# Optimization experiments

Measured on AMD Instinct MI355X. Metric: run time of the kernel, lower is better.

Reference implementation:

```python
import jax, jax.numpy as jnp
import numpy as np

N = 50000          # nodes
E = 800000         # edges
IN = 32            # in_channels (train_tensor.shape[1])
OUT = 256          # out_channels
K = 4              # Chebyshev order
LAMBDA_MAX = 2.0   # canonical lambda_max for sym-normalized Laplacian


def setup_inputs() -> dict:
    key = jax.random.key(0)
    ks = jax.random.split(key, 32)
    inp = {}
    inp["X"] = jax.random.normal(ks[0], (N, IN), jnp.float32)
    inp["edge_index"] = jax.random.randint(ks[1], (2, E), 0, N)
    inp["edge_weight"] = jax.random.uniform(ks[2], (E,), jnp.float32)
    inp["H"] = jax.random.normal(ks[3], (N, OUT), jnp.float32)
    inp["C"] = jax.random.normal(ks[4], (N, OUT), jnp.float32)
    i = 5
    s_in = float(np.sqrt(6.0 / (IN + OUT)))   # glorot for W_g
    s_ch = float(np.sqrt(1.0 / OUT))          # ChebConv linear init scale
    for g in ["i", "f", "c", "o"]:
        inp[f"W_{g}"] = jax.random.uniform(ks[i], (IN, OUT), jnp.float32, -s_in, s_in); i += 1
        inp[f"b_{g}"] = jnp.zeros((1, OUT), jnp.float32)
        inp[f"conv_{g}_w"] = jax.random.uniform(ks[i], (K, OUT, OUT), jnp.float32, -s_ch, s_ch); i += 1
        inp[f"conv_{g}_b"] = jnp.zeros((OUT,), jnp.float32)
    return inp


def _cheb_basis(H, edge_index, edge_weight, lam):
    """Chebyshev basis T_0(L~)H .. T_{K-1}(L~)H for the scaled sym Laplacian.
    L~ = (2/lam) * (I - D^{-1/2} A D^{-1/2}) - I  (PyG ChebConv.__norm__)."""
    n = H.shape[0]
    src, dst = edge_index[0], edge_index[1]
    deg = jax.ops.segment_sum(edge_weight, src, num_segments=n)
    dis = jnp.where(deg > 0, jax.lax.rsqrt(deg), 0.0)
    w = -(2.0 / lam) * dis[src] * edge_weight * dis[dst]   # scaled off-diagonal
    d = 2.0 / lam - 1.0                                     # scaled diagonal

    def prop(x):  # L~ @ x via edge scatter + diagonal
        return jax.ops.segment_sum(w[:, None] * x[src], dst, num_segments=n) + d * x

    Tx0 = H
    Tx1 = prop(Tx0)
    Tx2 = 2.0 * prop(Tx1) - Tx0
    Tx3 = 2.0 * prop(Tx2) - Tx1
    return jnp.stack([Tx0, Tx1, Tx2, Tx3])  # [K, N, OUT]


def reference(X, edge_index, edge_weight, H, C,
              W_i, b_i, conv_i_w, conv_i_b,
              W_f, b_f, conv_f_w, conv_f_b,
              W_c, b_c, conv_c_w, conv_c_b,
              W_o, b_o, conv_o_w, conv_o_b):
    # Shared Chebyshev basis of H (identical across the 4 gates)
    Tx = _cheb_basis(H, edge_index, edge_weight, LAMBDA_MAX)  # [K, N, OUT]

    def gate(Wg, bg, cw, cb):
        conv = jnp.einsum('knf,kfo->no', Tx, cw) + cb
        return X @ Wg + conv + bg

    I = jax.nn.sigmoid(gate(W_i, b_i, conv_i_w, conv_i_b))
    F = jax.nn.sigmoid(gate(W_f, b_f, conv_f_w, conv_f_b))
    T = jnp.tanh(gate(W_c, b_c, conv_c_w, conv_c_b))
    C_new = F * C + I * T
    O = jax.nn.sigmoid(gate(W_o, b_o, conv_o_w, conv_o_b))
    H_new = O * jnp.tanh(C_new)
    return (H_new, C_new)
```

## Files before the change

### kernel.cpp

```cpp
#include <hip/hip_runtime.h>
#include <math.h>

#define NN   50000
#define EE   800000
#define INC  32
#define OUTC 256
#define NKB  132

using bf16x8 = __attribute__((ext_vector_type(8))) short;
using u16x8  = __attribute__((ext_vector_type(8))) unsigned short;
using f32x4  = __attribute__((ext_vector_type(4))) float;

struct __align__(8) Edge { int s; float w; };

__device__ __forceinline__ unsigned short f2b(float f) {
  union { float f; unsigned u; } v; v.f = f;
  return (unsigned short)((v.u + 0x7FFFu + ((v.u >> 16) & 1u)) >> 16);
}
__device__ __forceinline__ float b2f(unsigned short u) {
  union { unsigned u; float f; } v; v.u = ((unsigned)u) << 16; return v.f;
}


__global__ void k_edge1(const int* __restrict__ ei, const float* __restrict__ ew,
                        float* __restrict__ deg, int* __restrict__ cnt) {
  for (int e = blockIdx.x * blockDim.x + threadIdx.x; e < EE;
       e += gridDim.x * blockDim.x) {
    atomicAdd(&deg[ei[e]], ew[e]);
    atomicAdd(&cnt[ei[EE + e]], 1);
  }
}

__global__ __launch_bounds__(512) void k_scan1(const int* __restrict__ cnt,
                                               int* __restrict__ row_ptr,
                                               int* __restrict__ bsum) {
  __shared__ int sd[512];
  int t = threadIdx.x;
  int i = blockIdx.x * 512 + t;
  int x = (i < NN) ? cnt[i] : 0;
  sd[t] = x;
  __syncthreads();
  for (int off = 1; off < 512; off <<= 1) {
    int v = (t >= off) ? sd[t - off] : 0;
    __syncthreads();
    sd[t] += v;
    __syncthreads();
  }
  if (i < NN) row_ptr[i] = sd[t] - x;
  if (t == 511) bsum[blockIdx.x] = sd[511];
}

__global__ __launch_bounds__(128) void k_scan2(int* __restrict__ bsum,
                                               int* __restrict__ row_ptr,
                                               int nblk) {
  __shared__ int sd[128];
  int t = threadIdx.x;
  int x = (t < nblk) ? bsum[t] : 0;
  sd[t] = x;
  __syncthreads();
  for (int off = 1; off < 128; off <<= 1) {
    int v = (t >= off) ? sd[t - off] : 0;
    __syncthreads();
    sd[t] += v;
    __syncthreads();
  }
  if (t < nblk) bsum[t] = sd[t] - x;
  if (t == 127) row_ptr[NN] = sd[127];
}

__global__ void k_scan3(int* __restrict__ row_ptr, const int* __restrict__ bsum,
                        int* __restrict__ nxt, float* __restrict__ deg) {
  int i = blockIdx.x * blockDim.x + threadIdx.x;
  if (i < NN) {
    int v = row_ptr[i] + bsum[i >> 9];
    row_ptr[i] = v;
    nxt[i] = v;
    float d = deg[i];
    deg[i] = d > 0.f ? rsqrtf(d) : 0.f;
  }
}

__global__ void k_fill(const int* __restrict__ ei, const float* __restrict__ ew,
                       const float* __restrict__ dis, int* __restrict__ nxt,
                       Edge* __restrict__ ev) {
  for (int e = blockIdx.x * blockDim.x + threadIdx.x; e < EE;
       e += gridDim.x * blockDim.x) {
    int s = ei[e], d = ei[EE + e];
    int pos = atomicAdd(&nxt[d], 1);
    Edge eg; eg.s = s; eg.w = -dis[s] * ew[e] * dis[d];
    ev[pos] = eg;
  }
}


__global__ __launch_bounds__(256) void k_prop_bf(
    const int* __restrict__ row_ptr, const Edge* __restrict__ ev,
    const unsigned short* __restrict__ xb,
    const unsigned short* __restrict__ initb, float scale,
    unsigned short* __restrict__ outb) {
  int wid = blockIdx.x * 4 + (threadIdx.x >> 6);
  if (wid >= NN) return;
  int lane = threadIdx.x & 63;
  int half = lane >> 5;
  int cl = lane & 31;
  int start = __builtin_amdgcn_readfirstlane(row_ptr[wid]);
  int end = __builtin_amdgcn_readfirstlane(row_ptr[wid + 1]);
  const size_t cofs = (size_t)(cl << 3);

  float a0[8], a1[8], a2[8], a3[8];
#pragma unroll
  for (int i = 0; i < 8; ++i) { a0[i] = 0.f; a1[i] = 0.f; a2[i] = 0.f; a3[i] = 0.f; }

  int j = start;
  for (; j + 7 < end; j += 8) {
    Edge e0 = ev[j + half];
    Edge e1 = ev[j + 2 + half];
    Edge e2 = ev[j + 4 + half];
    Edge e3 = ev[j + 6 + half];
    u16x8 u0 = *(const u16x8*)(xb + (size_t)e0.s * OUTC + cofs);
    u16x8 u1 = *(const u16x8*)(xb + (size_t)e1.s * OUTC + cofs);
    u16x8 u2 = *(const u16x8*)(xb + (size_t)e2.s * OUTC + cofs);
    u16x8 u3 = *(const u16x8*)(xb + (size_t)e3.s * OUTC + cofs);
#pragma unroll
    for (int i = 0; i < 8; ++i) {
      a0[i] = fmaf(e0.w, b2f(u0[i]), a0[i]);
      a1[i] = fmaf(e1.w, b2f(u1[i]), a1[i]);
      a2[i] = fmaf(e2.w, b2f(u2[i]), a2[i]);
      a3[i] = fmaf(e3.w, b2f(u3[i]), a3[i]);
    }
  }
  for (; j + 1 < end; j += 2) {
    Edge e0 = ev[j + half];
    u16x8 u0 = *(const u16x8*)(xb + (size_t)e0.s * OUTC + cofs);
#pragma unroll
    for (int i = 0; i < 8; ++i) a0[i] = fmaf(e0.w, b2f(u0[i]), a0[i]);
  }
  if (j < end) {
    Edge e0 = ev[j];
    float wv = half ? 0.f : e0.w;
    u16x8 u0 = *(const u16x8*)(xb + (size_t)e0.s * OUTC + cofs);
#pragma unroll
    for (int i = 0; i < 8; ++i) a0[i] = fmaf(wv, b2f(u0[i]), a0[i]);
  }

  float o[8];
#pragma unroll
  for (int i = 0; i < 8; ++i) {
    float s = (a0[i] + a1[i]) + (a2[i] + a3[i]);
    s += __shfl_xor(s, 32);
    o[i] = s;
  }
  if (initb) {
    u16x8 iv = *(const u16x8*)(initb + (size_t)wid * OUTC + cofs);
#pragma unroll
    for (int i = 0; i < 8; ++i) o[i] = scale * o[i] - b2f(iv[i]);
  }
  if (half == 1) {
    u16x8 h;
#pragma unroll
    for (int i = 0; i < 8; ++i) h[i] = f2b(o[i]);
    *(u16x8*)(outb + (size_t)wid * OUTC + cofs) = h;
  }
}


__global__ void k_packXH(const float* __restrict__ X, const float* __restrict__ H,
                         unsigned short* __restrict__ xrm,
                         unsigned short* __restrict__ hrm) {
  int t = blockIdx.x * blockDim.x + threadIdx.x;
  if (t < NN * 4) {
    int row = t >> 2, kb = t & 3;
    float4 a = *(const float4*)(X + (size_t)row * INC + kb * 8);
    float4 b = *(const float4*)(X + (size_t)row * INC + kb * 8 + 4);
    u16x8 h;
    h[0] = f2b(a.x); h[1] = f2b(a.y); h[2] = f2b(a.z); h[3] = f2b(a.w);
    h[4] = f2b(b.x); h[5] = f2b(b.y); h[6] = f2b(b.z); h[7] = f2b(b.w);
    *(u16x8*)(xrm + (size_t)row * INC + kb * 8) = h;
  } else if (t < NN * 36) {
    int u = t - NN * 4;
    int row = u >> 5, kb = u & 31;
    float4 a = *(const float4*)(H + (size_t)row * OUTC + kb * 8);
    float4 b = *(const float4*)(H + (size_t)row * OUTC + kb * 8 + 4);
    u16x8 h;
    h[0] = f2b(a.x); h[1] = f2b(a.y); h[2] = f2b(a.z); h[3] = f2b(a.w);
    h[4] = f2b(b.x); h[5] = f2b(b.y); h[6] = f2b(b.z); h[7] = f2b(b.w);
    *(u16x8*)(hrm + (size_t)row * OUTC + kb * 8) = h;
  }
}

struct BPtrs {
  const float* W[4];
  const float* cw[4];
  const float* b[4];
  const float* cb[4];
};

__global__ void k_packB(BPtrs bp, unsigned short* __restrict__ bpk,
                        float* __restrict__ bias_pk) {
  int t = blockIdx.x * blockDim.x + threadIdx.x;
  if (t >= NKB * 1024) return;
  int kb = t >> 10, p = t & 1023;
  int j = p >> 7, c = (p >> 6) & 1, g = (p >> 4) & 3, s = p & 15;
  int o = j * 32 + c * 16 + s;
  u16x8 h;
#pragma unroll
  for (int j8 = 0; j8 < 8; ++j8) {
    int k = kb * 8 + j8;
    float v = (k < 32) ? bp.W[g][k * OUTC + o]
                       : bp.cw[g][(size_t)(k - 32) * OUTC + o];
    h[j8] = f2b(v);
  }
  *(u16x8*)(bpk + (size_t)t * 8) = h;
  if (kb == 0) bias_pk[p] = bp.b[g][o] + bp.cb[g][o];
}


__device__ __forceinline__ float sigf(float x) {
  return __builtin_amdgcn_rcpf(1.0f + __expf(-x));
}
__device__ __forceinline__ float tanhfast(float x) {
  float e = __expf(2.0f * x);
  return 1.0f - 2.0f * __builtin_amdgcn_rcpf(e + 1.0f);
}

#define AS1(p) ((__attribute__((address_space(1))) void*)(p))
#define AS3(p) ((__attribute__((address_space(3))) void*)(p))

__global__ __launch_bounds__(512, 6) void k_gemm_mfma(
    const unsigned short* __restrict__ Xrm,
    const unsigned short* __restrict__ Hrm,
    const unsigned short* __restrict__ T1rm,
    const unsigned short* __restrict__ T2rm,
    const unsigned short* __restrict__ T3rm,
    const unsigned short* __restrict__ Bpk,
    const float* __restrict__ bias_pk,
    const float* __restrict__ C,
    float* __restrict__ Hn, float* __restrict__ Cn) {
  __shared__ unsigned short Als[3][128 * 4 * 8];
  __shared__ unsigned short Bls[3][4 * 128 * 8];

  const int b = blockIdx.x;
  const int xcd = b & 7;
  const int slot = b >> 3;
  const int cgrp = slot & 7;
  const int rblk = xcd + ((slot >> 3) << 3);
  const int bm0 = rblk * 128;
  if (bm0 >= NN) return;
  const int cb0 = cgrp * 128;

  const int tid = threadIdx.x;
  const int lane = tid & 63;
  const int wid = tid >> 6;
  const int wr = wid >> 1;
  const int wc = wid & 1;

  f32x4 acc[2][4];
#pragma unroll
  for (int i = 0; i < 2; ++i)
#pragma unroll
    for (int j = 0; j < 4; ++j) acc[i][j] = (f32x4){0.f, 0.f, 0.f, 0.f};

  const int sr = lane >> 2;
  const int scs = (lane & 3) ^ ((sr >> 1) & 3);
  int arow = bm0 + (wid << 4) + sr;
  if (arow > NN - 1) arow = NN - 1;
  const size_t rowA32 = (size_t)arow * INC + ((size_t)scs << 3);
  const size_t rowA256 = (size_t)arow * OUTC + ((size_t)scs << 3);
  const int idxw = wid << 6;
  const unsigned short* bG =
      Bpk + (((size_t)(idxw >> 7)) * 1024 + cb0 + (idxw & 127) + lane) * 8;

  auto STAGE_A = [&](int buf, int tile) {
    const unsigned short* src;
    if (tile == 0)      src = Xrm + rowA32;
    else if (tile < 9)  src = Hrm  + rowA256 + (size_t)(tile - 1) * 32;
    else if (tile < 17) src = T1rm + rowA256 + (size_t)(tile - 9) * 32;
    else if (tile < 25) src = T2rm + rowA256 + (size_t)(tile - 17) * 32;
    else                src = T3rm + rowA256 + (size_t)(tile - 25) * 32;
    __builtin_amdgcn_global_load_lds(AS1(src),
                                     AS3(&Als[buf][wid << 9]), 16, 0, 0);
  };
  auto STAGE_B = [&](int buf, int tile) {
    __builtin_amdgcn_global_load_lds(AS1(bG + ((size_t)(tile << 2)) * 1024 * 8),
                                     AS3(&Bls[buf][(wid << 6) * 8]), 16, 0, 0);
  };

  const int koff = lane >> 4;
  const int r15 = lane & 15;
  const int NT = NKB / 4;

  STAGE_A(0, 0); STAGE_B(0, 0);
  STAGE_A(1, 1); STAGE_B(1, 1);
  int cur = 0;
  for (int t = 0; t < NT; ++t) {
    if (t < NT - 1)
      asm volatile("s_waitcnt vmcnt(2)\n\ts_barrier" ::: "memory");
    else
      asm volatile("s_waitcnt vmcnt(0)\n\ts_barrier" ::: "memory");

    const int row0 = (wr << 5) + r15;
    const int asw = (r15 >> 1) & 3;
    const unsigned short* Ab = &Als[cur][row0 * 32 + ((koff ^ asw) << 3)];
    const unsigned short* Bb = &Bls[cur][((koff << 7) + (wc << 6) + r15) * 8];

    bf16x8 af0 = *(const bf16x8*)(Ab);
    bf16x8 af1 = *(const bf16x8*)(Ab + 512);
    bf16x8 bf0 = *(const bf16x8*)(Bb + 0 * 8);
    bf16x8 bf1 = *(const bf16x8*)(Bb + 16 * 8);
    bf16x8 bf2 = *(const bf16x8*)(Bb + 32 * 8);
    bf16x8 bf3 = *(const bf16x8*)(Bb + 48 * 8);
    if (t + 2 < NT) { STAGE_A((t + 2) % 3, t + 2); STAGE_B((t + 2) % 3, t + 2); }
    __builtin_amdgcn_s_barrier();
    asm volatile("s_waitcnt lgkmcnt(0)" ::: "memory");
    __builtin_amdgcn_sched_barrier(0);
    __builtin_amdgcn_s_setprio(1);
    acc[0][0] = __builtin_amdgcn_mfma_f32_16x16x32_bf16(af0, bf0, acc[0][0], 0, 0, 0);
    acc[1][0] = __builtin_amdgcn_mfma_f32_16x16x32_bf16(af1, bf0, acc[1][0], 0, 0, 0);
    acc[0][1] = __builtin_amdgcn_mfma_f32_16x16x32_bf16(af0, bf1, acc[0][1], 0, 0, 0);
    acc[1][1] = __builtin_amdgcn_mfma_f32_16x16x32_bf16(af1, bf1, acc[1][1], 0, 0, 0);
    acc[0][2] = __builtin_amdgcn_mfma_f32_16x16x32_bf16(af0, bf2, acc[0][2], 0, 0, 0);
    acc[1][2] = __builtin_amdgcn_mfma_f32_16x16x32_bf16(af1, bf2, acc[1][2], 0, 0, 0);
    acc[0][3] = __builtin_amdgcn_mfma_f32_16x16x32_bf16(af0, bf3, acc[0][3], 0, 0, 0);
    acc[1][3] = __builtin_amdgcn_mfma_f32_16x16x32_bf16(af1, bf3, acc[1][3], 0, 0, 0);
    __builtin_amdgcn_s_setprio(0);

    cur = (cur + 1 == 3) ? 0 : cur + 1;
  }

  const int ocol = cgrp * 32 + (wc << 4) + r15;
  float bz[4];
#pragma unroll
  for (int g = 0; g < 4; ++g) bz[g] = bias_pk[cb0 + (wc << 6) + (g << 4) + r15];

#pragma unroll
  for (int mi = 0; mi < 2; ++mi) {
    int rowb = bm0 + (wr << 5) + (mi << 4) + ((lane >> 4) << 2);
#pragma unroll
    for (int q = 0; q < 4; ++q) {
      int r = rowb + q;
      if (r >= NN) continue;
      float zi = acc[mi][0][q] + bz[0];
      float zf = acc[mi][1][q] + bz[1];
      float zc = acc[mi][2][q] + bz[2];
      float zo = acc[mi][3][q] + bz[3];
      float cold = C[(size_t)r * OUTC + ocol];
      float I = sigf(zi), F = sigf(zf), T = tanhfast(zc), O = sigf(zo);
      float cn = fmaf(F, cold, I * T);
      Cn[(size_t)r * OUTC + ocol] = cn;
      Hn[(size_t)r * OUTC + ocol] = O * tanhfast(cn);
    }
  }
}


extern "C" void kernel_launch(void* const* d_in, const int* in_sizes, int n_in,
                              void* d_out, int out_size, void* d_ws, size_t ws_size,
                              hipStream_t stream) {
  const float* X = (const float*)d_in[0];
  const int* EI = (const int*)d_in[1];
  const float* EW = (const float*)d_in[2];
  const float* H = (const float*)d_in[3];
  const float* C = (const float*)d_in[4];

  char* ws = (char*)d_ws;
  size_t off = 0;
  auto alloc = [&](size_t bytes) -> void* {
    void* p = ws + off;
    off += (bytes + 255) & ~(size_t)255;
    return p;
  };
  int* row_ptr = (int*)alloc((NN + 1) * sizeof(int));
  int* cnt = (int*)alloc(NN * sizeof(int));
  int* nextp = (int*)alloc(NN * sizeof(int));
  int* bsum = (int*)alloc(128 * sizeof(int));
  Edge* ev = (Edge*)alloc(EE * sizeof(Edge));
  float* dis = (float*)alloc(NN * sizeof(float));
  unsigned short* Xrm = (unsigned short*)alloc((size_t)NN * INC * sizeof(unsigned short));
  unsigned short* Hrm = (unsigned short*)alloc((size_t)NN * OUTC * sizeof(unsigned short));
  unsigned short* T1rm = (unsigned short*)alloc((size_t)NN * OUTC * sizeof(unsigned short));
  unsigned short* T2rm = (unsigned short*)alloc((size_t)NN * OUTC * sizeof(unsigned short));
  unsigned short* T3rm = (unsigned short*)alloc((size_t)NN * OUTC * sizeof(unsigned short));
  unsigned short* Bpk = (unsigned short*)alloc((size_t)NKB * 1024 * 8 * sizeof(unsigned short));
  float* bias_pk = (float*)alloc(1024 * sizeof(float));
  (void)ws_size; (void)in_sizes; (void)n_in; (void)out_size;

  hipMemsetAsync(dis, 0, NN * sizeof(float), stream);
  hipMemsetAsync(cnt, 0, NN * sizeof(int), stream);

  const int ge = 1024;
  k_edge1<<<ge, 256, 0, stream>>>(EI, EW, dis, cnt);
  const int nscb = (NN + 511) / 512;
  k_scan1<<<nscb, 512, 0, stream>>>(cnt, row_ptr, bsum);
  k_scan2<<<1, 128, 0, stream>>>(bsum, row_ptr, nscb);
  k_scan3<<<(NN + 255) / 256, 256, 0, stream>>>(row_ptr, bsum, nextp, dis);
  k_fill<<<ge, 256, 0, stream>>>(EI, EW, dis, nextp, ev);

  k_packXH<<<(NN * 36 + 255) / 256, 256, 0, stream>>>(X, H, Xrm, Hrm);
  BPtrs bp;
  for (int g = 0; g < 4; ++g) {
    bp.W[g] = (const float*)d_in[5 + 4 * g];
    bp.b[g] = (const float*)d_in[6 + 4 * g];
    bp.cw[g] = (const float*)d_in[7 + 4 * g];
    bp.cb[g] = (const float*)d_in[8 + 4 * g];
  }
  k_packB<<<(NKB * 1024 + 255) / 256, 256, 0, stream>>>(bp, Bpk, bias_pk);

  const int pgrid = (NN + 3) / 4;
  k_prop_bf<<<pgrid, 256, 0, stream>>>(row_ptr, ev, Hrm, nullptr, 1.f, T1rm);
  k_prop_bf<<<pgrid, 256, 0, stream>>>(row_ptr, ev, T1rm, Hrm, 2.f, T2rm);
  k_prop_bf<<<pgrid, 256, 0, stream>>>(row_ptr, ev, T2rm, T1rm, 2.f, T3rm);

  float* Hn = (float*)d_out;
  float* Cn = (float*)d_out + (size_t)NN * OUTC;
  k_gemm_mfma<<<8 * 49 * 8, 512, 0, stream>>>(Xrm, Hrm, T1rm, T2rm, T3rm,
                                              Bpk, bias_pk, C, Hn, Cn);
}
```

Baseline: 490.7 us.

## Tile activations into 32-column panels and propagate per column tile

Activations (X, H, T1..T3) move into one buffer laid out as 33 contiguous panels of N×32 bf16. The propagation kernel now handles one 32-column tile per block group across 8 passes, with 8 edges in flight per wave, so each gather touches a compact 3.2MB panel that can stay in cache. The GEMM A-staging becomes a single strided address per tile. The trade-off is that the edge list and row pointers are re-read once per column tile, and each gather moves only 8 bytes, at the cost of more shuffles and wave-level reductions.

```diff
diff --git a/kernel.cpp b/kernel.cpp
--- a/kernel.cpp
+++ b/kernel.cpp
@@ -6,9 +6,11 @@
 #define INC  32
 #define OUTC 256
 #define NKB  132
+#define PNB  6250
 
 using bf16x8 = __attribute__((ext_vector_type(8))) short;
 using u16x8  = __attribute__((ext_vector_type(8))) unsigned short;
+using u16x4  = __attribute__((ext_vector_type(4))) unsigned short;
 using f32x4  = __attribute__((ext_vector_type(4))) float;
 
 struct __align__(8) Edge { int s; float w; };
@@ -93,80 +95,69 @@
 }
 
 
-__global__ __launch_bounds__(256) void k_prop_bf(
+__global__ __launch_bounds__(512) void k_prop_ct(
     const int* __restrict__ row_ptr, const Edge* __restrict__ ev,
-    const unsigned short* __restrict__ xb,
-    const unsigned short* __restrict__ initb, float scale,
-    unsigned short* __restrict__ outb) {
-  int wid = blockIdx.x * 4 + (threadIdx.x >> 6);
-  if (wid >= NN) return;
-  int lane = threadIdx.x & 63;
-  int half = lane >> 5;
-  int cl = lane & 31;
-  int start = __builtin_amdgcn_readfirstlane(row_ptr[wid]);
-  int end = __builtin_amdgcn_readfirstlane(row_ptr[wid + 1]);
-  const size_t cofs = (size_t)(cl << 3);
-
-  float a0[8], a1[8], a2[8], a3[8];
-#pragma unroll
-  for (int i = 0; i < 8; ++i) { a0[i] = 0.f; a1[i] = 0.f; a2[i] = 0.f; a3[i] = 0.f; }
-
-  int j = start;
-  for (; j + 7 < end; j += 8) {
-    Edge e0 = ev[j + half];
-    Edge e1 = ev[j + 2 + half];
-    Edge e2 = ev[j + 4 + half];
-    Edge e3 = ev[j + 6 + half];
-    u16x8 u0 = *(const u16x8*)(xb + (size_t)e0.s * OUTC + cofs);
-    u16x8 u1 = *(const u16x8*)(xb + (size_t)e1.s * OUTC + cofs);
-    u16x8 u2 = *(const u16x8*)(xb + (size_t)e2.s * OUTC + cofs);
-    u16x8 u3 = *(const u16x8*)(xb + (size_t)e3.s * OUTC + cofs);
-#pragma unroll
-    for (int i = 0; i < 8; ++i) {
-      a0[i] = fmaf(e0.w, b2f(u0[i]), a0[i]);
-      a1[i] = fmaf(e1.w, b2f(u1[i]), a1[i]);
-      a2[i] = fmaf(e2.w, b2f(u2[i]), a2[i]);
-      a3[i] = fmaf(e3.w, b2f(u3[i]), a3[i]);
-    }
-  }
-  for (; j + 1 < end; j += 2) {
-    Edge e0 = ev[j + half];
-    u16x8 u0 = *(const u16x8*)(xb + (size_t)e0.s * OUTC + cofs);
-#pragma unroll
-    for (int i = 0; i < 8; ++i) a0[i] = fmaf(e0.w, b2f(u0[i]), a0[i]);
+    unsigned short* __restrict__ Actm,
+    int xp0, int ip0, float scale, int op0) {
+  const int bx = blockIdx.x;
+  const int ct = bx / PNB;
+  const int nb = bx - ct * PNB;
+  const int node = nb * 8 + (threadIdx.x >> 6);
+  const int lane = threadIdx.x & 63;
+  const int eslot = lane >> 3;
+  const int cg = lane & 7;
+  const int start = __builtin_amdgcn_readfirstlane(row_ptr[node]);
+  const int end = __builtin_amdgcn_readfirstlane(row_ptr[node + 1]);
+  const unsigned short* src = Actm + (size_t)(xp0 + ct) * (NN * 32) + (cg << 2);
+
+  float a0 = 0.f, a1 = 0.f, a2 = 0.f, a3 = 0.f;
+  int j = start + eslot;
+  for (; j < end - 8; j += 16) {
+    Edge e0 = ev[j];
+    Edge e1 = ev[j + 8];
+    u16x4 u0 = *(const u16x4*)(src + (size_t)e0.s * 32);
+    u16x4 u1 = *(const u16x4*)(src + (size_t)e1.s * 32);
+    a0 = fmaf(e0.w, b2f(u0[0]), a0);
+    a1 = fmaf(e0.w, b2f(u0[1]), a1);
+    a2 = fmaf(e0.w, b2f(u0[2]), a2);
+    a3 = fmaf(e0.w, b2f(u0[3]), a3);
+    a0 = fmaf(e1.w, b2f(u1[0]), a0);
+    a1 = fmaf(e1.w, b2f(u1[1]), a1);
+    a2 = fmaf(e1.w, b2f(u1[2]), a2);
+    a3 = fmaf(e1.w, b2f(u1[3]), a3);
   }
   if (j < end) {
     Edge e0 = ev[j];
-    float wv = half ? 0.f : e0.w;
-    u16x8 u0 = *(const u16x8*)(xb + (size_t)e0.s * OUTC + cofs);
-#pragma unroll
-    for (int i = 0; i < 8; ++i) a0[i] = fmaf(wv, b2f(u0[i]), a0[i]);
-  }
-
-  float o[8];
-#pragma unroll
-  for (int i = 0; i < 8; ++i) {
-    float s = (a0[i] + a1[i]) + (a2[i] + a3[i]);
-    s += __shfl_xor(s, 32);
-    o[i] = s;
-  }
-  if (initb) {
-    u16x8 iv = *(const u16x8*)(initb + (size_t)wid * OUTC + cofs);
-#pragma unroll
-    for (int i = 0; i < 8; ++i) o[i] = scale * o[i] - b2f(iv[i]);
-  }
-  if (half == 1) {
-    u16x8 h;
-#pragma unroll
-    for (int i = 0; i < 8; ++i) h[i] = f2b(o[i]);
-    *(u16x8*)(outb + (size_t)wid * OUTC + cofs) = h;
+    u16x4 u0 = *(const u16x4*)(src + (size_t)e0.s * 32);
+    a0 = fmaf(e0.w, b2f(u0[0]), a0);
+    a1 = fmaf(e0.w, b2f(u0[1]), a1);
+    a2 = fmaf(e0.w, b2f(u0[2]), a2);
+    a3 = fmaf(e0.w, b2f(u0[3]), a3);
+  }
+  a0 += __shfl_xor(a0, 8);  a1 += __shfl_xor(a1, 8);
+  a2 += __shfl_xor(a2, 8);  a3 += __shfl_xor(a3, 8);
+  a0 += __shfl_xor(a0, 16); a1 += __shfl_xor(a1, 16);
+  a2 += __shfl_xor(a2, 16); a3 += __shfl_xor(a3, 16);
+  a0 += __shfl_xor(a0, 32); a1 += __shfl_xor(a1, 32);
+  a2 += __shfl_xor(a2, 32); a3 += __shfl_xor(a3, 32);
+
+  if (lane < 8) {
+    if (ip0 >= 0) {
+      u16x4 iv = *(const u16x4*)(Actm + ((size_t)(ip0 + ct) * NN + node) * 32 + (lane << 2));
+      a0 = scale * a0 - b2f(iv[0]);
+      a1 = scale * a1 - b2f(iv[1]);
+      a2 = scale * a2 - b2f(iv[2]);
+      a3 = scale * a3 - b2f(iv[3]);
+    }
+    u16x4 h;
+    h[0] = f2b(a0); h[1] = f2b(a1); h[2] = f2b(a2); h[3] = f2b(a3);
+    *(u16x4*)(Actm + ((size_t)(op0 + ct) * NN + node) * 32 + (lane << 2)) = h;
   }
 }
 
 
 __global__ void k_packXH(const float* __restrict__ X, const float* __restrict__ H,
-                         unsigned short* __restrict__ xrm,
-                         unsigned short* __restrict__ hrm) {
+                         unsigned short* __restrict__ Actm) {
   int t = blockIdx.x * blockDim.x + threadIdx.x;
   if (t < NN * 4) {
     int row = t >> 2, kb = t & 3;
@@ -175,16 +166,17 @@
     u16x8 h;
     h[0] = f2b(a.x); h[1] = f2b(a.y); h[2] = f2b(a.z); h[3] = f2b(a.w);
     h[4] = f2b(b.x); h[5] = f2b(b.y); h[6] = f2b(b.z); h[7] = f2b(b.w);
-    *(u16x8*)(xrm + (size_t)row * INC + kb * 8) = h;
+    *(u16x8*)(Actm + (size_t)row * 32 + kb * 8) = h;
   } else if (t < NN * 36) {
     int u = t - NN * 4;
     int row = u >> 5, kb = u & 31;
+    int ct = kb >> 2, pc = kb & 3;
     float4 a = *(const float4*)(H + (size_t)row * OUTC + kb * 8);
     float4 b = *(const float4*)(H + (size_t)row * OUTC + kb * 8 + 4);
     u16x8 h;
     h[0] = f2b(a.x); h[1] = f2b(a.y); h[2] = f2b(a.z); h[3] = f2b(a.w);
     h[4] = f2b(b.x); h[5] = f2b(b.y); h[6] = f2b(b.z); h[7] = f2b(b.w);
-    *(u16x8*)(hrm + (size_t)row * OUTC + kb * 8) = h;
+    *(u16x8*)(Actm + ((size_t)(1 + ct) * NN + row) * 32 + pc * 8) = h;
   }
 }
 
@@ -227,11 +219,7 @@
 #define AS3(p) ((__attribute__((address_space(3))) void*)(p))
 
 __global__ __launch_bounds__(512, 6) void k_gemm_mfma(
-    const unsigned short* __restrict__ Xrm,
-    const unsigned short* __restrict__ Hrm,
-    const unsigned short* __restrict__ T1rm,
-    const unsigned short* __restrict__ T2rm,
-    const unsigned short* __restrict__ T3rm,
+    const unsigned short* __restrict__ Actm,
     const unsigned short* __restrict__ Bpk,
     const float* __restrict__ bias_pk,
     const float* __restrict__ C,
@@ -264,21 +252,15 @@
   const int scs = (lane & 3) ^ ((sr >> 1) & 3);
   int arow = bm0 + (wid << 4) + sr;
   if (arow > NN - 1) arow = NN - 1;
-  const size_t rowA32 = (size_t)arow * INC + ((size_t)scs << 3);
-  const size_t rowA256 = (size_t)arow * OUTC + ((size_t)scs << 3);
+  const size_t rowoff = (size_t)arow * 32 + ((size_t)scs << 3);
   const int idxw = wid << 6;
   const unsigned short* bG =
       Bpk + (((size_t)(idxw >> 7)) * 1024 + cb0 + (idxw & 127) + lane) * 8;
 
   auto STAGE_A = [&](int buf, int tile) {
-    const unsigned short* src;
-    if (tile == 0)      src = Xrm + rowA32;
-    else if (tile < 9)  src = Hrm  + rowA256 + (size_t)(tile - 1) * 32;
-    else if (tile < 17) src = T1rm + rowA256 + (size_t)(tile - 9) * 32;
-    else if (tile < 25) src = T2rm + rowA256 + (size_t)(tile - 17) * 32;
-    else                src = T3rm + rowA256 + (size_t)(tile - 25) * 32;
-    __builtin_amdgcn_global_load_lds(AS1(src),
-                                     AS3(&Als[buf][wid << 9]), 16, 0, 0);
+    __builtin_amdgcn_global_load_lds(
+        AS1(Actm + (size_t)tile * (NN * 32) + rowoff),
+        AS3(&Als[buf][wid << 9]), 16, 0, 0);
   };
   auto STAGE_B = [&](int buf, int tile) {
     __builtin_amdgcn_global_load_lds(AS1(bG + ((size_t)(tile << 2)) * 1024 * 8),
@@ -375,11 +357,7 @@
   int* bsum = (int*)alloc(128 * sizeof(int));
   Edge* ev = (Edge*)alloc(EE * sizeof(Edge));
   float* dis = (float*)alloc(NN * sizeof(float));
-  unsigned short* Xrm = (unsigned short*)alloc((size_t)NN * INC * sizeof(unsigned short));
-  unsigned short* Hrm = (unsigned short*)alloc((size_t)NN * OUTC * sizeof(unsigned short));
-  unsigned short* T1rm = (unsigned short*)alloc((size_t)NN * OUTC * sizeof(unsigned short));
-  unsigned short* T2rm = (unsigned short*)alloc((size_t)NN * OUTC * sizeof(unsigned short));
-  unsigned short* T3rm = (unsigned short*)alloc((size_t)NN * OUTC * sizeof(unsigned short));
+  unsigned short* Actm = (unsigned short*)alloc((size_t)33 * NN * 32 * sizeof(unsigned short));
   unsigned short* Bpk = (unsigned short*)alloc((size_t)NKB * 1024 * 8 * sizeof(unsigned short));
   float* bias_pk = (float*)alloc(1024 * sizeof(float));
   (void)ws_size; (void)in_sizes; (void)n_in; (void)out_size;
@@ -395,7 +373,7 @@
   k_scan3<<<(NN + 255) / 256, 256, 0, stream>>>(row_ptr, bsum, nextp, dis);
   k_fill<<<ge, 256, 0, stream>>>(EI, EW, dis, nextp, ev);
 
-  k_packXH<<<(NN * 36 + 255) / 256, 256, 0, stream>>>(X, H, Xrm, Hrm);
+  k_packXH<<<(NN * 36 + 255) / 256, 256, 0, stream>>>(X, H, Actm);
   BPtrs bp;
   for (int g = 0; g < 4; ++g) {
     bp.W[g] = (const float*)d_in[5 + 4 * g];
@@ -405,13 +383,11 @@
   }
   k_packB<<<(NKB * 1024 + 255) / 256, 256, 0, stream>>>(bp, Bpk, bias_pk);
 
-  const int pgrid = (NN + 3) / 4;
-  k_prop_bf<<<pgrid, 256, 0, stream>>>(row_ptr, ev, Hrm, nullptr, 1.f, T1rm);
-  k_prop_bf<<<pgrid, 256, 0, stream>>>(row_ptr, ev, T1rm, Hrm, 2.f, T2rm);
-  k_prop_bf<<<pgrid, 256, 0, stream>>>(row_ptr, ev, T2rm, T1rm, 2.f, T3rm);
+  k_prop_ct<<<8 * PNB, 512, 0, stream>>>(row_ptr, ev, Actm, 1, -1, 1.f, 9);
+  k_prop_ct<<<8 * PNB, 512, 0, stream>>>(row_ptr, ev, Actm, 9, 1, 2.f, 17);
+  k_prop_ct<<<8 * PNB, 512, 0, stream>>>(row_ptr, ev, Actm, 17, 9, 2.f, 25);
 
   float* Hn = (float*)d_out;
   float* Cn = (float*)d_out + (size_t)NN * OUTC;
-  k_gemm_mfma<<<8 * 49 * 8, 512, 0, stream>>>(Xrm, Hrm, T1rm, T2rm, T3rm,
-                                              Bpk, bias_pk, C, Hn, Cn);
-}
+  k_gemm_mfma<<<8 * 49 * 8, 512, 0, stream>>>(Actm, Bpk, bias_pk, C, Hn, Cn);
+}
```

New measurement: 704.6 us. 43.6% more time.
